# Performance work log

Measured on AMD Instinct MI355X. Metric: run time of the kernel, lower is better.

The kernel has to match this reference:

```python
import jax, jax.numpy as jnp
import numpy as np

B, L, D_IN, H, N2, NL, D_OUT = 32, 4096, 16, 128, 32, 4, 8


def setup_inputs() -> dict:
    key = jax.random.key(0)
    ks = jax.random.split(key, 12)
    x = jax.random.normal(ks[0], (B, L, D_IN), jnp.float32)
    times = jax.random.uniform(ks[1], (B, L), jnp.float32)
    enc_w = jax.random.normal(ks[2], (H, D_IN), jnp.float32) / np.sqrt(D_IN)
    enc_b = jnp.zeros((H,), jnp.float32)
    # S4D kernel params per layer (stacked along NL)
    log_dt = jax.random.uniform(ks[3], (NL, H), jnp.float32) * (np.log(0.1) - np.log(0.001)) + np.log(0.001)
    log_A_real = jnp.full((NL, H, N2), np.log(0.5), jnp.float32)
    A_imag = jnp.broadcast_to(np.pi * jnp.arange(N2, dtype=jnp.float32), (NL, H, N2)).astype(jnp.float32)
    C_re = jax.random.normal(ks[4], (NL, H, N2), jnp.float32) * (0.5 ** 0.5)
    C_im = jax.random.normal(ks[5], (NL, H, N2), jnp.float32) * (0.5 ** 0.5)
    D = jax.random.normal(ks[6], (NL, H), jnp.float32)
    conv_w = jax.random.normal(ks[7], (NL, 2 * H, H), jnp.float32) / np.sqrt(H)  # 1x1 conv
    conv_b = jnp.zeros((NL, 2 * H), jnp.float32)
    ln_w = jnp.ones((NL, H), jnp.float32)
    ln_b = jnp.zeros((NL, H), jnp.float32)
    dec_w = jax.random.normal(ks[8], (D_OUT, H), jnp.float32) / np.sqrt(H)
    dec_b = jnp.zeros((D_OUT,), jnp.float32)
    return dict(x=x, times=times, enc_w=enc_w, enc_b=enc_b, log_dt=log_dt,
                log_A_real=log_A_real, A_imag=A_imag, C_re=C_re, C_im=C_im, D=D,
                conv_w=conv_w, conv_b=conv_b, ln_w=ln_w, ln_b=ln_b, dec_w=dec_w, dec_b=dec_b)


def _s4d_kernel(log_dt, log_A_real, A_imag, C_re, C_im, L_):
    # Vandermonde construction of the S4D convolution kernel, shape (H, L)
    dt = jnp.exp(log_dt)[:, None]                      # (H, 1)
    A = -jnp.exp(log_A_real) + 1j * A_imag             # (H, N2)
    dtA = A * dt                                       # (H, N2)
    C = (C_re + 1j * C_im) * (jnp.exp(dtA) - 1.0) / A  # (H, N2)
    K = jnp.exp(dtA[:, :, None] * jnp.arange(L_))      # (H, N2, L)
    return 2.0 * jnp.einsum('hn,hnl->hl', C, K).real


def _layernorm(x, w, b, eps=1e-5):
    mu = x.mean(-1, keepdims=True)
    var = ((x - mu) ** 2).mean(-1, keepdims=True)
    return (x - mu) * jax.lax.rsqrt(var + eps) * w + b


def _forward(x, enc_w, enc_b, log_dt, log_A_real, A_imag, C_re, C_im, D,
             conv_w, conv_b, ln_w, ln_b, dec_w, dec_b):
    L_ = x.shape[1]
    u = jnp.transpose(x @ enc_w.T + enc_b, (0, 2, 1))  # (B, H, L)
    for l in range(NL):
        z = u
        k = _s4d_kernel(log_dt[l], log_A_real[l], A_imag[l], C_re[l], C_im[l], L_)  # (H, L)
        # FFT-based causal convolution with zero padding to 2L
        k_f = jnp.fft.rfft(k, n=2 * L_)                # (H, L+1)
        u_f = jnp.fft.rfft(z, n=2 * L_)                # (B, H, L+1)
        y = jnp.fft.irfft(u_f * k_f, n=2 * L_)[..., :L_]
        y = y + z * D[l][:, None]                      # skip term
        y = jax.nn.gelu(y, approximate=False)          # torch nn.GELU = exact erf
        # 1x1 conv to 2H channels then GLU over channel dim
        v = jnp.einsum('oh,bhl->bol', conv_w[l], y) + conv_b[l][:, None]
        a, g = jnp.split(v, 2, axis=1)
        y = a * jax.nn.sigmoid(g)
        u = y + u                                      # residual
        u = jnp.transpose(_layernorm(jnp.transpose(u, (0, 2, 1)), ln_w[l], ln_b[l]), (0, 2, 1))  # postnorm
    emb = jnp.transpose(u, (0, 2, 1))                  # (B, L, H)
    pooled = emb.mean(axis=1)                          # (B, H)
    pred = jax.nn.sigmoid(pooled @ dec_w.T + dec_b)    # (B, D_OUT)
    return pred, emb


def reference(x, times, enc_w, enc_b, log_dt, log_A_real, A_imag, C_re, C_im, D,
              conv_w, conv_b, ln_w, ln_b, dec_w, dec_b):
    # times is accepted but unused, matching the original forward signature
    return _forward(x, enc_w, enc_b, log_dt, log_A_real, A_imag, C_re, C_im, D,
                    conv_w, conv_b, ln_w, ln_b, dec_w, dec_b)
```

## Files before the change

### kernel.cpp

```cpp
#include <hip/hip_runtime.h>
#include <hip/hip_bf16.h>

#define B_ 32
#define L_ 4096
#define DIN 16
#define H_ 128
#define N2_ 32
#define NL_ 4
#define CL 64
#define NC 64

#define OFF_U   ((size_t)0)
#define SZ_U    ((size_t)B_*H_*L_/2)
#define OFF_Y   (OFF_U + SZ_U)
#define SZ_Y    ((size_t)B_*H_*L_/2)
#define OFF_K   (OFF_Y + SZ_Y)
#define SZ_K    ((size_t)NL_*H_*64)
#define OFF_CP  (OFF_K + SZ_K)
#define SZ_CP   ((size_t)NL_*H_*64)
#define OFF_W64 (OFF_CP + SZ_CP)
#define SZ_W64  ((size_t)NL_*H_*64)
#define OFF_W5  (OFF_W64 + SZ_W64)
#define SZ_W5   ((size_t)NL_*H_*64)
#define OFF_DTA (OFF_W5 + SZ_W5)
#define SZ_DTA  ((size_t)NL_*H_*N2_*4)
#define OFF_PL  (OFF_DTA + SZ_DTA)
#define SZ_PL   ((size_t)B_*H_)
#define OFF_WB  (OFF_PL + SZ_PL)
#define SZ_WB   ((size_t)NL_*256*128/2)
#define OFF_T1F (OFF_WB + SZ_WB)
#define SZ_TF   ((size_t)NL_*H_*4096)
#define OFF_TKF (OFF_T1F + SZ_TF)
#define OFF_T2F (OFF_TKF + SZ_TF)

#define ZP 72
#define EP 68

typedef __bf16 bf16_t;
typedef bf16_t bf16x8 __attribute__((ext_vector_type(8)));
typedef float f32x4 __attribute__((ext_vector_type(4)));
typedef unsigned short u16x8 __attribute__((ext_vector_type(8)));

#define MFMA(a, b, c) __builtin_amdgcn_mfma_f32_16x16x32_bf16(a, b, c, 0, 0, 0)
#define BCB(v) __builtin_bit_cast(bf16x8, v)

__device__ __forceinline__ unsigned short f2bf(float f) {
    return __builtin_bit_cast(unsigned short, (__bf16)f);
}
__device__ __forceinline__ float bf2f(unsigned short u) {
    return __builtin_bit_cast(float, (unsigned int)u << 16);
}
__device__ __forceinline__ void store_hl(unsigned short* p, int idx, float v) {
    unsigned short hi = f2bf(v);
    p[idx]     = hi;
    p[idx + 8] = f2bf(v - bf2f(hi));
}
__device__ __forceinline__ float gelu_f(float a) {
    float uu = a * fmaf(0.0356774081f, a * a, 0.7978845608f);
    float e  = __expf(2.0f * uu);
    float th = 1.0f - 2.0f / (e + 1.0f);
    return 0.5f * a * (1.0f + th);
}
__device__ __forceinline__ int yswz(int l, int h) {
    return (l * 128 + h) ^ ((l & 7) << 3);
}

__global__ __launch_bounds__(256) void prep_params(const float* log_dt, const float* log_A_real,
                                                   const float* A_imag, const float* C_re,
                                                   const float* C_im, float* ws) {
    int idx = blockIdx.x * 256 + threadIdx.x;
    if (idx >= NL_ * H_ * N2_) return;
    int n  = idx & 31;
    int lh = idx >> 5;

    float dt  = expf(log_dt[lh]);
    float Are = -expf(log_A_real[idx]);
    float Aim = A_imag[idx];
    float dre = Are * dt, dim = Aim * dt;
    float er  = expf(dre);
    float sw, cw; sincosf(dim, &sw, &cw);
    float wre = er * cw, wim = er * sw;
    float nre = wre - 1.0f, nim = wim;
    float den = Are * Are + Aim * Aim;
    float qre = (nre * Are + nim * Aim) / den;
    float qim = (nim * Are - nre * Aim) / den;
    float cre = C_re[idx], cim = C_im[idx];

    float* cp  = ws + OFF_CP  + (size_t)lh * 64;
    float* w64 = ws + OFF_W64 + (size_t)lh * 64;
    float* w5  = ws + OFF_W5  + (size_t)lh * 64;
    cp[2 * n]     = cre * qre - cim * qim;
    cp[2 * n + 1] = cre * qim + cim * qre;
    *((float4*)(ws + OFF_DTA) + (size_t)lh * 32 + n) = make_float4(dre, dim, wre, wim);

    float e64 = expf(64.0f * dre);
    float s64, c64; sincosf(64.0f * dim, &s64, &c64);
    float ar = e64 * c64, ai = e64 * s64;
    w64[2 * n] = ar; w64[2 * n + 1] = ai;
    #pragma unroll
    for (int q = 0; q < 3; ++q) {
        float nr = ar * ar - ai * ai;
        float ni = 2.0f * ar * ai;
        ar = nr; ai = ni;
    }
    w5[2 * n] = ar; w5[2 * n + 1] = ai;
}

__global__ __launch_bounds__(256) void prep_pow(float* ws) {
    int idx = blockIdx.x * 256 + threadIdx.x;
    int n  = idx & 31;
    int e  = (idx >> 5) & 63;
    int lh = idx >> 11;
    float4 dw = *((const float4*)(ws + OFF_DTA) + (size_t)lh * 32 + n);
    float ew = expf((float)e * dw.x);
    float sn, cs; sincosf((float)e * dw.y, &sn, &cs);
    float pr = ew * cs, pi = ew * sn;

    unsigned short* t1f = (unsigned short*)(ws + OFF_T1F) + (size_t)lh * 8192;
    unsigned short* t2f = (unsigned short*)(ws + OFF_T2F) + (size_t)lh * 8192;
    int k1 = 63 - e;
    store_hl(t1f, (k1 >> 3) * 1024 + (2 * n) * 16 + (k1 & 7), pr);
    store_hl(t1f, (k1 >> 3) * 1024 + (2 * n + 1) * 16 + (k1 & 7), pi);
    float qr = pr * dw.z - pi * dw.w;
    float qi = pr * dw.w + pi * dw.z;
    store_hl(t2f, ((2 * n) >> 3) * 1024 + e * 16 + ((2 * n) & 7), qr);
    store_hl(t2f, ((2 * n + 1) >> 3) * 1024 + e * 16 + ((2 * n + 1) & 7), qi);
}

__global__ __launch_bounds__(256) void compute_k(float* ws) {
    int idx = blockIdx.x * 256 + threadIdx.x;
    if (idx >= NL_ * H_ * 64) return;
    int s  = idx & 63;
    int lh = idx >> 6;
    const float* cp = ws + OFF_CP + (size_t)lh * 64;
    const float4* dta = (const float4*)(ws + OFF_DTA) + (size_t)lh * 32;
    float acc = 0.0f;
    #pragma unroll 8
    for (int n = 0; n < 32; ++n) {
        float4 dw = dta[n];
        float ew = expf((float)s * dw.x);
        float sn, cs; sincosf((float)s * dw.y, &sn, &cs);
        acc += cp[2 * n] * (ew * cs) - cp[2 * n + 1] * (ew * sn);
    }
    ws[OFF_K + (size_t)lh * 64 + s] = 2.0f * acc;
}

__global__ __launch_bounds__(256) void prep_tkf(float* ws) {
    int idx = blockIdx.x * 256 + threadIdx.x;
    int tau = idx & 63;
    int s   = (idx >> 6) & 63;
    int lh  = idx >> 12;
    float v = (tau >= s) ? ws[OFF_K + (size_t)lh * 64 + (tau - s)] : 0.0f;
    unsigned short* dst = (unsigned short*)(ws + OFF_TKF) + (size_t)lh * 8192;
    store_hl(dst, (s >> 3) * 1024 + (s & 7) + tau * 16, v);
}

__global__ __launch_bounds__(256) void prep_wbf(const float* conv_w, float* ws) {
    int i = blockIdx.x * 256 + threadIdx.x;
    ((unsigned short*)(ws + OFF_WB))[i] = f2bf(conv_w[i]);
}

__global__ __launch_bounds__(256) void encoder_kernel(const float* x, const float* enc_w,
                                                      const float* enc_b, float* ws) {
    __shared__ float wlds[H_ * DIN];
    __shared__ float blds[H_];
    int t  = threadIdx.x;
    int b  = blockIdx.x >> 4;
    int l0 = (blockIdx.x & 15) * 256;
    for (int i = t; i < H_ * DIN; i += 256) wlds[i] = enc_w[i];
    if (t < H_) blds[t] = enc_b[t];
    float xr[16];
    const float* xp = x + ((size_t)b * L_ + l0 + t) * DIN;
    #pragma unroll
    for (int d = 0; d < 16; ++d) xr[d] = xp[d];
    __syncthreads();
    unsigned short* u = (unsigned short*)(ws + OFF_U) + (size_t)b * H_ * L_ + l0 + t;
    for (int h = 0; h < H_; ++h) {
        float acc = blds[h];
        #pragma unroll
        for (int d = 0; d < 16; ++d) acc += xr[d] * wlds[h * 16 + d];
        u[(size_t)h * L_] = f2bf(acc);
    }
}

__global__ __launch_bounds__(256) void s4d_mfma(const float* Dp, float* ws, int layer) {
    __shared__ unsigned short zsh[64 * ZP];
    __shared__ float eg[64 * EP];
    __shared__ float tex[8][64];
    __shared__ float bex[8][64];

    int t  = threadIdx.x;
    int b  = blockIdx.x >> 7;
    int h  = blockIdx.x & 127;
    int lh = layer * H_ + h;
    int w  = t >> 6;
    int l  = t & 63;
    int lr = l & 15;
    int lg = l >> 4;

    const unsigned short* ug = (const unsigned short*)(ws + OFF_U) + ((size_t)b * H_ + h) * L_;

    {
        int base = t * 16;
        int c = base >> 6, s0 = base & 63;
        *(u16x8*)&zsh[c * ZP + s0]     = *(const u16x8*)&ug[base];
        *(u16x8*)&zsh[c * ZP + s0 + 8] = *(const u16x8*)&ug[base + 8];
    }

    const unsigned short* t1f = (const unsigned short*)(ws + OFF_T1F) + (size_t)lh * 8192;
    const unsigned short* tkf = (const unsigned short*)(ws + OFF_TKF) + (size_t)lh * 8192;
    const unsigned short* t2f = (const unsigned short*)(ws + OFF_T2F) + (size_t)lh * 8192;
    int bo = lg * 1024 + (w * 16 + lr) * 16;
    bf16x8 T1h0 = BCB(*(const u16x8*)&t1f[bo]);
    bf16x8 T1l0 = BCB(*(const u16x8*)&t1f[bo + 8]);
    bf16x8 T1h1 = BCB(*(const u16x8*)&t1f[bo + 4096]);
    bf16x8 T1l1 = BCB(*(const u16x8*)&t1f[bo + 4096 + 8]);
    bf16x8 TKh0 = BCB(*(const u16x8*)&tkf[bo]);
    bf16x8 TKl0 = BCB(*(const u16x8*)&tkf[bo + 8]);
    bf16x8 TKh1 = BCB(*(const u16x8*)&tkf[bo + 4096]);
    bf16x8 TKl1 = BCB(*(const u16x8*)&tkf[bo + 4096 + 8]);

    f32x4 accE[4], accC[4];
    #pragma unroll
    for (int ct = 0; ct < 4; ++ct) { accE[ct] = (f32x4)0.0f; accC[ct] = (f32x4)0.0f; }

    __syncthreads();

    #pragma unroll
    for (int ct = 0; ct < 4; ++ct) {
        int ar = (ct * 16 + lr) * ZP;
        bf16x8 ah0 = BCB(*(const u16x8*)&zsh[ar + lg * 8]);
        bf16x8 ah1 = BCB(*(const u16x8*)&zsh[ar + 32 + lg * 8]);
        accE[ct] = MFMA(ah0, T1h0, accE[ct]);
        accE[ct] = MFMA(ah0, T1l0, accE[ct]);
        accE[ct] = MFMA(ah1, T1h1, accE[ct]);
        accE[ct] = MFMA(ah1, T1l1, accE[ct]);
        accC[ct] = MFMA(ah0, TKh0, accC[ct]);
        accC[ct] = MFMA(ah0, TKl0, accC[ct]);
        accC[ct] = MFMA(ah1, TKh1, accC[ct]);
        accC[ct] = MFMA(ah1, TKl1, accC[ct]);
    }
    #pragma unroll
    for (int ct = 0; ct < 4; ++ct)
        #pragma unroll
        for (int r = 0; r < 4; ++r)
            eg[(ct * 16 + lg * 4 + r) * EP + w * 16 + lr] = accE[ct][r];

    bf16x8 T2h0 = BCB(*(const u16x8*)&t2f[bo]);
    bf16x8 T2l0 = BCB(*(const u16x8*)&t2f[bo + 8]);
    bf16x8 T2h1 = BCB(*(const u16x8*)&t2f[bo + 4096]);
    bf16x8 T2l1 = BCB(*(const u16x8*)&t2f[bo + 4096 + 8]);
    float zep[16];
    #pragma unroll
    for (int ct = 0; ct < 4; ++ct)
        #pragma unroll
        for (int r = 0; r < 4; ++r) {
            int c = ct * 16 + lg * 4 + r, tau = w * 16 + lr;
            zep[ct * 4 + r] = bf2f(zsh[c * ZP + tau]);
        }
    __syncthreads();

    {
        int n   = t & 31;
        int oct = t >> 5;
        const float* cp   = ws + OFF_CP  + (size_t)lh * 64;
        const float* w64p = ws + OFF_W64 + (size_t)lh * 64;
        const float* w5p  = ws + OFF_W5  + (size_t)lh * 64;
        float cre = cp[2 * n], cim = cp[2 * n + 1];
        float wr  = w64p[2 * n], wi = w64p[2 * n + 1];
        float2 e[8];
        float sre = 0.f, sim = 0.f;
        #pragma unroll
        for (int j = 0; j < 8; ++j) {
            e[j] = *(const float2*)&eg[(8 * oct + j) * EP + 2 * n];
            float nr = fmaf(wr, sre, fmaf(-wi, sim, e[j].x));
            float ni = fmaf(wr, sim, fmaf(wi, sre, e[j].y));
            sre = nr; sim = ni;
        }
        *(float2*)&tex[oct][2 * n] = make_float2(sre, sim);
        __syncthreads();
        if (t < 32) {
            float Wr = w5p[2 * n], Wi = w5p[2 * n + 1];
            float br = 0.f, bi = 0.f;
            #pragma unroll
            for (int o = 0; o < 8; ++o) {
                *(float2*)&bex[o][2 * n] = make_float2(br, bi);
                float2 T = *(const float2*)&tex[o][2 * n];
                float nr = fmaf(Wr, br, fmaf(-Wi, bi, T.x));
                float ni = fmaf(Wr, bi, fmaf(Wi, br, T.y));
                br = nr; bi = ni;
            }
        }
        __syncthreads();
        float2 Sb = *(const float2*)&bex[oct][2 * n];
        sre = Sb.x; sim = Sb.y;
        #pragma unroll
        for (int j = 0; j < 8; ++j) {
            int c = 8 * oct + j;
            float gre = 2.0f * (cre * sre - cim * sim);
            float gim = -2.0f * (cre * sim + cim * sre);
            unsigned int pk = (unsigned int)f2bf(gre) | ((unsigned int)f2bf(gim) << 16);
            *(unsigned int*)&zsh[c * ZP + 2 * n] = pk;
            float nr = fmaf(wr, sre, fmaf(-wi, sim, e[j].x));
            float ni = fmaf(wr, sim, fmaf(wi, sre, e[j].y));
            sre = nr; sim = ni;
        }
    }
    float Dh = Dp[lh];
    __syncthreads();

    #pragma unroll
    for (int ct = 0; ct < 4; ++ct) {
        int ar = (ct * 16 + lr) * ZP;
        bf16x8 gh0 = BCB(*(const u16x8*)&zsh[ar + lg * 8]);
        bf16x8 gh1 = BCB(*(const u16x8*)&zsh[ar + 32 + lg * 8]);
        accC[ct] = MFMA(gh0, T2h0, accC[ct]);
        accC[ct] = MFMA(gh0, T2l0, accC[ct]);
        accC[ct] = MFMA(gh1, T2h1, accC[ct]);
        accC[ct] = MFMA(gh1, T2l1, accC[ct]);
    }

    unsigned short* yb = (unsigned short*)(ws + OFF_Y) + ((size_t)b * H_ + h) * L_;
    #pragma unroll
    for (int ct = 0; ct < 4; ++ct)
        #pragma unroll
        for (int r = 0; r < 4; ++r) {
            float acc = fmaf(Dh, zep[ct * 4 + r], accC[ct][r]);
            yb[(ct * 16 + lg * 4 + r) * 64 + w * 16 + lr] = f2bf(gelu_f(acc));
        }
}

__global__ __launch_bounds__(256) void conv_glu_ln_mfma(const float* conv_b, const float* ln_w,
                                                        const float* ln_b, float* ws, float* outp,
                                                        int layer, int last) {
    __shared__ unsigned short yt[64 * 128];
    __shared__ float wsum[4][64];
    __shared__ float wsq[4][64];

    int t    = threadIdx.x;
    int b    = blockIdx.x >> 6;
    int l0   = (blockIdx.x & 63) * 64;
    int w    = t >> 6;
    int lam  = t & 63;
    int g4   = lam >> 4;
    int ncol = lam & 15;

    const unsigned short* yg = (const unsigned short*)(ws + OFF_Y) + (size_t)b * H_ * L_;
    const unsigned short* wb = (const unsigned short*)(ws + OFF_WB) + (size_t)layer * 256 * 128;

    {
        int ll = t & 63;
        int hb = (t >> 6) * 32;
        const unsigned short* ycol = yg + l0 + ll;
        #pragma unroll
        for (int g = 0; g < 4; ++g) {
            u16x8 tmp;
            #pragma unroll
            for (int i = 0; i < 8; ++i)
                tmp[i] = ycol[(size_t)(hb + g * 8 + i) * L_];
            *(u16x8*)&yt[yswz(ll, hb + g * 8)] = tmp;
        }
    }

    const float* cb = conv_b + layer * 256;
    f32x4 dA[2][4], dG[2][4];
    #pragma unroll
    for (int oa = 0; oa < 2; ++oa) {
        int ba = w * 32 + oa * 16 + g4 * 4;
        f32x4 bA, bG;
        #pragma unroll
        for (int r = 0; r < 4; ++r) { bA[r] = cb[ba + r]; bG[r] = cb[128 + ba + r]; }
        #pragma unroll
        for (int nt = 0; nt < 4; ++nt) { dA[oa][nt] = bA; dG[oa][nt] = bG; }
    }
    __syncthreads();

    #pragma unroll
    for (int kt = 0; kt < 4; ++kt) {
        bf16x8 aAk[2], aGk[2];
        #pragma unroll
        for (int oa = 0; oa < 2; ++oa) {
            int oA = w * 32 + oa * 16 + ncol;
            aAk[oa] = BCB(*(const u16x8*)&wb[(size_t)oA * 128 + kt * 32 + g4 * 8]);
            aGk[oa] = BCB(*(const u16x8*)&wb[(size_t)(128 + oA) * 128 + kt * 32 + g4 * 8]);
        }
        #pragma unroll
        for (int nt = 0; nt < 4; ++nt) {
            bf16x8 bfr = BCB(*(const u16x8*)&yt[yswz(nt * 16 + ncol, kt * 32 + g4 * 8)]);
            #pragma unroll
            for (int oa = 0; oa < 2; ++oa) {
                dA[oa][nt] = MFMA(aAk[oa], bfr, dA[oa][nt]);
                dG[oa][nt] = MFMA(aGk[oa], bfr, dG[oa][nt]);
            }
        }
    }

    unsigned short* ug = (unsigned short*)(ws + OFF_U) + (size_t)b * H_ * L_;
    float lwv[2][4], lbv[2][4];
    #pragma unroll
    for (int oa = 0; oa < 2; ++oa)
        #pragma unroll
        for (int r = 0; r < 4; ++r) {
            int hh = layer * 128 + w * 32 + oa * 16 + g4 * 4 + r;
            lwv[oa][r] = ln_w[hh]; lbv[oa][r] = ln_b[hh];
        }

    #pragma unroll
    for (int nt = 0; nt < 4; ++nt) {
        int l = l0 + nt * 16 + ncol;
        float s = 0.f, q = 0.f;
        #pragma unroll
        for (int oa = 0; oa < 2; ++oa)
            #pragma unroll
            for (int r = 0; r < 4; ++r) {
                int h = w * 32 + oa * 16 + g4 * 4 + r;
                float a = dA[oa][nt][r], g = dG[oa][nt][r];
                float val = a / (1.0f + __expf(-g)) + bf2f(ug[(size_t)h * L_ + l]);
                dA[oa][nt][r] = val;
                s += val; q += val * val;
            }
        s += __shfl_xor(s, 16, 64); q += __shfl_xor(q, 16, 64);
        s += __shfl_xor(s, 32, 64); q += __shfl_xor(q, 32, 64);
        if (g4 == 0) { wsum[w][nt * 16 + ncol] = s; wsq[w][nt * 16 + ncol] = q; }
    }
    __syncthreads();

    #pragma unroll
    for (int nt = 0; nt < 4; ++nt) {
        int ll = nt * 16 + ncol;
        int l  = l0 + ll;
        float S = wsum[0][ll] + wsum[1][ll] + wsum[2][ll] + wsum[3][ll];
        float Q = wsq[0][ll] + wsq[1][ll] + wsq[2][ll] + wsq[3][ll];
        float mu = S * (1.0f / 128.0f);
        float var = Q * (1.0f / 128.0f) - mu * mu;
        float rstd = rsqrtf(var + 1e-5f);
        #pragma unroll
        for (int oa = 0; oa < 2; ++oa) {
            float vv[4];
            #pragma unroll
            for (int r = 0; r < 4; ++r) {
                int h = w * 32 + oa * 16 + g4 * 4 + r;
                float v = (dA[oa][nt][r] - mu) * rstd * lwv[oa][r] + lbv[oa][r];
                vv[r] = v;
                ug[(size_t)h * L_ + l] = f2bf(v);
            }
            if (last) {
                *(float4*)&outp[((size_t)(b * L_ + l)) * H_ + w * 32 + oa * 16 + g4 * 4] =
                    make_float4(vv[0], vv[1], vv[2], vv[3]);
            }
        }
    }
}

__global__ __launch_bounds__(256) void pool_kernel(float* ws) {
    int bh = blockIdx.x;
    const unsigned short* u = (const unsigned short*)(ws + OFF_U) + (size_t)bh * L_;
    int t = threadIdx.x;
    float s = 0.0f;
    for (int i = t; i < L_; i += 256) s += bf2f(u[i]);
    #pragma unroll
    for (int m = 1; m <= 32; m <<= 1) s += __shfl_xor(s, m, 64);
    __shared__ float part[4];
    if ((t & 63) == 0) part[t >> 6] = s;
    __syncthreads();
    if (t == 0) ws[OFF_PL + bh] = (part[0] + part[1] + part[2] + part[3]) * (1.0f / L_);
}

__global__ __launch_bounds__(256) void decode_kernel(const float* dec_w, const float* dec_b,
                                                     const float* ws, float* out) {
    int t = threadIdx.x;
    int b = t >> 3, o = t & 7;
    const float* p = ws + OFF_PL + b * 128;
    float acc = dec_b[o];
    for (int h = 0; h < 128; ++h) acc += p[h] * dec_w[o * 128 + h];
    out[t] = 1.0f / (1.0f + __expf(-acc));
}

extern "C" void kernel_launch(void* const* d_in, const int* in_sizes, int n_in,
                              void* d_out, int out_size, void* d_ws, size_t ws_size,
                              hipStream_t stream) {
    const float* x          = (const float*)d_in[0];
    const float* enc_w      = (const float*)d_in[2];
    const float* enc_b      = (const float*)d_in[3];
    const float* log_dt     = (const float*)d_in[4];
    const float* log_A_real = (const float*)d_in[5];
    const float* A_imag     = (const float*)d_in[6];
    const float* C_re       = (const float*)d_in[7];
    const float* C_im       = (const float*)d_in[8];
    const float* Dp         = (const float*)d_in[9];
    const float* conv_w     = (const float*)d_in[10];
    const float* conv_b     = (const float*)d_in[11];
    const float* ln_w       = (const float*)d_in[12];
    const float* ln_b       = (const float*)d_in[13];
    const float* dec_w      = (const float*)d_in[14];
    const float* dec_b      = (const float*)d_in[15];
    float* ws = (float*)d_ws;
    float* out = (float*)d_out;

    prep_params<<<(NL_ * H_ * N2_ + 255) / 256, 256, 0, stream>>>(log_dt, log_A_real, A_imag,
                                                                  C_re, C_im, ws);
    prep_pow<<<(NL_ * H_ * N2_ * 64) / 256, 256, 0, stream>>>(ws);
    compute_k<<<(NL_ * H_ * 64 + 255) / 256, 256, 0, stream>>>(ws);
    prep_tkf<<<(NL_ * H_ * 64 * 64) / 256, 256, 0, stream>>>(ws);
    prep_wbf<<<(NL_ * 256 * 128) / 256, 256, 0, stream>>>(conv_w, ws);
    encoder_kernel<<<B_ * (L_ / 256), 256, 0, stream>>>(x, enc_w, enc_b, ws);
    for (int l = 0; l < NL_; ++l) {
        s4d_mfma<<<B_ * H_, 256, 0, stream>>>(Dp, ws, l);
        conv_glu_ln_mfma<<<B_ * (L_ / 64), 256, 0, stream>>>(conv_b, ln_w, ln_b, ws,
                                                             out + 256, l, l == NL_ - 1);
    }
    pool_kernel<<<B_ * H_, 256, 0, stream>>>(ws);
    decode_kernel<<<1, 256, 0, stream>>>(dec_w, dec_b, ws, out);
}
```

Before: 355.3 us.

## Process two L-tiles per block in conv-GLU-LN, prefetching next Y tile into registers

Each conv_glu_ln block now handles 128 sequence positions as two 64-wide tiles instead of one. The second tile's Y data is loaded from global memory into registers while the first tile's MFMA and epilogue run, then written to shared memory after a barrier. The aim is to hide the strided global gather latency behind compute. In exchange the grid is halved to 1024 blocks, which lowers parallelism and adds an extra barrier and register pressure.

```diff
diff --git a/kernel.cpp b/kernel.cpp
--- a/kernel.cpp
+++ b/kernel.cpp
@@ -338,64 +338,20 @@
     __shared__ float wsq[4][64];
 
     int t    = threadIdx.x;
-    int b    = blockIdx.x >> 6;
-    int l0   = (blockIdx.x & 63) * 64;
+    int b    = blockIdx.x >> 5;
+    int lbp  = blockIdx.x & 31;
     int w    = t >> 6;
     int lam  = t & 63;
     int g4   = lam >> 4;
     int ncol = lam & 15;
+    int ll   = t & 63;
+    int hbs  = (t >> 6) * 32;
 
     const unsigned short* yg = (const unsigned short*)(ws + OFF_Y) + (size_t)b * H_ * L_;
     const unsigned short* wb = (const unsigned short*)(ws + OFF_WB) + (size_t)layer * 256 * 128;
-
-    {
-        int ll = t & 63;
-        int hb = (t >> 6) * 32;
-        const unsigned short* ycol = yg + l0 + ll;
-        #pragma unroll
-        for (int g = 0; g < 4; ++g) {
-            u16x8 tmp;
-            #pragma unroll
-            for (int i = 0; i < 8; ++i)
-                tmp[i] = ycol[(size_t)(hb + g * 8 + i) * L_];
-            *(u16x8*)&yt[yswz(ll, hb + g * 8)] = tmp;
-        }
-    }
-
+    unsigned short* ug = (unsigned short*)(ws + OFF_U) + (size_t)b * H_ * L_;
     const float* cb = conv_b + layer * 256;
-    f32x4 dA[2][4], dG[2][4];
-    #pragma unroll
-    for (int oa = 0; oa < 2; ++oa) {
-        int ba = w * 32 + oa * 16 + g4 * 4;
-        f32x4 bA, bG;
-        #pragma unroll
-        for (int r = 0; r < 4; ++r) { bA[r] = cb[ba + r]; bG[r] = cb[128 + ba + r]; }
-        #pragma unroll
-        for (int nt = 0; nt < 4; ++nt) { dA[oa][nt] = bA; dG[oa][nt] = bG; }
-    }
-    __syncthreads();
-
-    #pragma unroll
-    for (int kt = 0; kt < 4; ++kt) {
-        bf16x8 aAk[2], aGk[2];
-        #pragma unroll
-        for (int oa = 0; oa < 2; ++oa) {
-            int oA = w * 32 + oa * 16 + ncol;
-            aAk[oa] = BCB(*(const u16x8*)&wb[(size_t)oA * 128 + kt * 32 + g4 * 8]);
-            aGk[oa] = BCB(*(const u16x8*)&wb[(size_t)(128 + oA) * 128 + kt * 32 + g4 * 8]);
-        }
-        #pragma unroll
-        for (int nt = 0; nt < 4; ++nt) {
-            bf16x8 bfr = BCB(*(const u16x8*)&yt[yswz(nt * 16 + ncol, kt * 32 + g4 * 8)]);
-            #pragma unroll
-            for (int oa = 0; oa < 2; ++oa) {
-                dA[oa][nt] = MFMA(aAk[oa], bfr, dA[oa][nt]);
-                dG[oa][nt] = MFMA(aGk[oa], bfr, dG[oa][nt]);
-            }
-        }
-    }
-
-    unsigned short* ug = (unsigned short*)(ws + OFF_U) + (size_t)b * H_ * L_;
+
     float lwv[2][4], lbv[2][4];
     #pragma unroll
     for (int oa = 0; oa < 2; ++oa)
@@ -405,50 +361,120 @@
             lwv[oa][r] = ln_w[hh]; lbv[oa][r] = ln_b[hh];
         }
 
-    #pragma unroll
-    for (int nt = 0; nt < 4; ++nt) {
-        int l = l0 + nt * 16 + ncol;
-        float s = 0.f, q = 0.f;
-        #pragma unroll
-        for (int oa = 0; oa < 2; ++oa)
-            #pragma unroll
-            for (int r = 0; r < 4; ++r) {
-                int h = w * 32 + oa * 16 + g4 * 4 + r;
-                float a = dA[oa][nt][r], g = dG[oa][nt][r];
-                float val = a / (1.0f + __expf(-g)) + bf2f(ug[(size_t)h * L_ + l]);
-                dA[oa][nt][r] = val;
-                s += val; q += val * val;
+    u16x8 sr[4];
+    {
+        const unsigned short* ycol = yg + lbp * 128 + ll;
+        #pragma unroll
+        for (int g = 0; g < 4; ++g) {
+            u16x8 tmp;
+            #pragma unroll
+            for (int i = 0; i < 8; ++i)
+                tmp[i] = ycol[(size_t)(hbs + g * 8 + i) * L_];
+            sr[g] = tmp;
+        }
+        #pragma unroll
+        for (int g = 0; g < 4; ++g) *(u16x8*)&yt[yswz(ll, hbs + g * 8)] = sr[g];
+    }
+    __syncthreads();
+
+    #pragma unroll 1
+    for (int tile = 0; tile < 2; ++tile) {
+        int l0 = lbp * 128 + tile * 64;
+
+        f32x4 dA[2][4], dG[2][4];
+        #pragma unroll
+        for (int oa = 0; oa < 2; ++oa) {
+            int ba = w * 32 + oa * 16 + g4 * 4;
+            f32x4 bA, bG;
+            #pragma unroll
+            for (int r = 0; r < 4; ++r) { bA[r] = cb[ba + r]; bG[r] = cb[128 + ba + r]; }
+            #pragma unroll
+            for (int nt = 0; nt < 4; ++nt) { dA[oa][nt] = bA; dG[oa][nt] = bG; }
+        }
+
+        #pragma unroll
+        for (int kt = 0; kt < 4; ++kt) {
+            bf16x8 aAk[2], aGk[2];
+            #pragma unroll
+            for (int oa = 0; oa < 2; ++oa) {
+                int oA = w * 32 + oa * 16 + ncol;
+                aAk[oa] = BCB(*(const u16x8*)&wb[(size_t)oA * 128 + kt * 32 + g4 * 8]);
+                aGk[oa] = BCB(*(const u16x8*)&wb[(size_t)(128 + oA) * 128 + kt * 32 + g4 * 8]);
             }
-        s += __shfl_xor(s, 16, 64); q += __shfl_xor(q, 16, 64);
-        s += __shfl_xor(s, 32, 64); q += __shfl_xor(q, 32, 64);
-        if (g4 == 0) { wsum[w][nt * 16 + ncol] = s; wsq[w][nt * 16 + ncol] = q; }
-    }
-    __syncthreads();
-
-    #pragma unroll
-    for (int nt = 0; nt < 4; ++nt) {
-        int ll = nt * 16 + ncol;
-        int l  = l0 + ll;
-        float S = wsum[0][ll] + wsum[1][ll] + wsum[2][ll] + wsum[3][ll];
-        float Q = wsq[0][ll] + wsq[1][ll] + wsq[2][ll] + wsq[3][ll];
-        float mu = S * (1.0f / 128.0f);
-        float var = Q * (1.0f / 128.0f) - mu * mu;
-        float rstd = rsqrtf(var + 1e-5f);
-        #pragma unroll
-        for (int oa = 0; oa < 2; ++oa) {
-            float vv[4];
-            #pragma unroll
-            for (int r = 0; r < 4; ++r) {
-                int h = w * 32 + oa * 16 + g4 * 4 + r;
-                float v = (dA[oa][nt][r] - mu) * rstd * lwv[oa][r] + lbv[oa][r];
-                vv[r] = v;
-                ug[(size_t)h * L_ + l] = f2bf(v);
+            #pragma unroll
+            for (int nt = 0; nt < 4; ++nt) {
+                bf16x8 bfr = BCB(*(const u16x8*)&yt[yswz(nt * 16 + ncol, kt * 32 + g4 * 8)]);
+                #pragma unroll
+                for (int oa = 0; oa < 2; ++oa) {
+                    dA[oa][nt] = MFMA(aAk[oa], bfr, dA[oa][nt]);
+                    dG[oa][nt] = MFMA(aGk[oa], bfr, dG[oa][nt]);
+                }
             }
-            if (last) {
-                *(float4*)&outp[((size_t)(b * L_ + l)) * H_ + w * 32 + oa * 16 + g4 * 4] =
-                    make_float4(vv[0], vv[1], vv[2], vv[3]);
+        }
+
+        if (tile == 0) {
+            const unsigned short* ycol = yg + lbp * 128 + 64 + ll;
+            #pragma unroll
+            for (int g = 0; g < 4; ++g) {
+                u16x8 tmp;
+                #pragma unroll
+                for (int i = 0; i < 8; ++i)
+                    tmp[i] = ycol[(size_t)(hbs + g * 8 + i) * L_];
+                sr[g] = tmp;
             }
         }
+
+        #pragma unroll
+        for (int nt = 0; nt < 4; ++nt) {
+            int l = l0 + nt * 16 + ncol;
+            float s = 0.f, q = 0.f;
+            #pragma unroll
+            for (int oa = 0; oa < 2; ++oa)
+                #pragma unroll
+                for (int r = 0; r < 4; ++r) {
+                    int h = w * 32 + oa * 16 + g4 * 4 + r;
+                    float a = dA[oa][nt][r], g = dG[oa][nt][r];
+                    float val = a / (1.0f + __expf(-g)) + bf2f(ug[(size_t)h * L_ + l]);
+                    dA[oa][nt][r] = val;
+                    s += val; q += val * val;
+                }
+            s += __shfl_xor(s, 16, 64); q += __shfl_xor(q, 16, 64);
+            s += __shfl_xor(s, 32, 64); q += __shfl_xor(q, 32, 64);
+            if (g4 == 0) { wsum[w][nt * 16 + ncol] = s; wsq[w][nt * 16 + ncol] = q; }
+        }
+        __syncthreads();
+
+        if (tile == 0) {
+            #pragma unroll
+            for (int g = 0; g < 4; ++g) *(u16x8*)&yt[yswz(ll, hbs + g * 8)] = sr[g];
+        }
+
+        #pragma unroll
+        for (int nt = 0; nt < 4; ++nt) {
+            int ll2 = nt * 16 + ncol;
+            int l   = l0 + ll2;
+            float S = wsum[0][ll2] + wsum[1][ll2] + wsum[2][ll2] + wsum[3][ll2];
+            float Q = wsq[0][ll2] + wsq[1][ll2] + wsq[2][ll2] + wsq[3][ll2];
+            float mu = S * (1.0f / 128.0f);
+            float var = Q * (1.0f / 128.0f) - mu * mu;
+            float rstd = rsqrtf(var + 1e-5f);
+            #pragma unroll
+            for (int oa = 0; oa < 2; ++oa) {
+                float vv[4];
+                #pragma unroll
+                for (int r = 0; r < 4; ++r) {
+                    int h = w * 32 + oa * 16 + g4 * 4 + r;
+                    float v = (dA[oa][nt][r] - mu) * rstd * lwv[oa][r] + lbv[oa][r];
+                    vv[r] = v;
+                    ug[(size_t)h * L_ + l] = f2bf(v);
+                }
+                if (last) {
+                    *(float4*)&outp[((size_t)(b * L_ + l)) * H_ + w * 32 + oa * 16 + g4 * 4] =
+                        make_float4(vv[0], vv[1], vv[2], vv[3]);
+                }
+            }
+        }
+        if (tile == 0) __syncthreads();
     }
 }
 
@@ -506,8 +532,8 @@
     encoder_kernel<<<B_ * (L_ / 256), 256, 0, stream>>>(x, enc_w, enc_b, ws);
     for (int l = 0; l < NL_; ++l) {
         s4d_mfma<<<B_ * H_, 256, 0, stream>>>(Dp, ws, l);
-        conv_glu_ln_mfma<<<B_ * (L_ / 64), 256, 0, stream>>>(conv_b, ln_w, ln_b, ws,
-                                                             out + 256, l, l == NL_ - 1);
+        conv_glu_ln_mfma<<<B_ * 32, 256, 0, stream>>>(conv_b, ln_w, ln_b, ws,
+                                                      out + 256, l, l == NL_ - 1);
     }
     pool_kernel<<<B_ * H_, 256, 0, stream>>>(ws);
     decode_kernel<<<1, 256, 0, stream>>>(dec_w, dec_b, ws, out);
```

Result: slower. 411.4 us (+15.8%).
